# Kernel optimization log

Measured on AMD Instinct MI355X. Metric: run time of the kernel, lower is better.

## Reference

```python
import jax, jax.numpy as jnp
import numpy as np

N_SRC = 100000
N_DST = 100000
E = 500000
D = 128
L = 2


def _sage(x_src, x_dst, e_src, e_dst, W_self, W_neigh, b):
    # DGL SAGEConv('mean'): out = x_dst @ W_self^T + mean_neighbors(x_src) @ W_neigh^T + b
    n_dst = x_dst.shape[0]
    msg_sum = jax.ops.segment_sum(x_src[e_src], e_dst, num_segments=n_dst)  # [n_dst, D]
    deg = jax.ops.segment_sum(jnp.ones((e_dst.shape[0],), x_src.dtype), e_dst, num_segments=n_dst)
    h_neigh = msg_sum / jnp.maximum(deg, 1.0)[:, None]  # isolated nodes -> 0
    return x_dst @ W_self.T + h_neigh @ W_neigh.T + b


def setup_inputs() -> dict:
    key = jax.random.key(0)
    ks = jax.random.split(key, 10)
    s = 1.0 / np.sqrt(D)
    return {
        "x_src": jax.random.normal(ks[0], (N_SRC, D), jnp.float32),
        "x_dst": jax.random.normal(ks[1], (N_DST, D), jnp.float32),
        "e_src": jax.random.randint(ks[2], (E,), 0, N_SRC, jnp.int32),
        "e_dst": jax.random.randint(ks[3], (E,), 0, N_DST, jnp.int32),
        "W_ship_self": jax.random.normal(ks[4], (L, D, D), jnp.float32) * s,
        "W_ship_neigh": jax.random.normal(ks[5], (L, D, D), jnp.float32) * s,
        "b_ship": jnp.zeros((L, D), jnp.float32),
        "W_rev_self": jax.random.normal(ks[6], (L, D, D), jnp.float32) * s,
        "W_rev_neigh": jax.random.normal(ks[7], (L, D, D), jnp.float32) * s,
        "b_rev": jnp.zeros((L, D), jnp.float32),
    }


def reference(x_src, x_dst, e_src, e_dst, W_ship_self, W_ship_neigh, b_ship,
              W_rev_self, W_rev_neigh, b_rev):
    h_s, h_d = x_src, x_dst
    n_layers = W_ship_self.shape[0]
    for l in range(n_layers):
        # ('source','ship','destination'): messages source -> destination
        new_d = _sage(h_s, h_d, e_src, e_dst, W_ship_self[l], W_ship_neigh[l], b_ship[l])
        # ('destination','rev_ship','source'): messages destination -> source
        new_s = _sage(h_d, h_s, e_dst, e_src, W_rev_self[l], W_rev_neigh[l], b_rev[l])
        h_d = jax.nn.relu(new_d)
        h_s = jax.nn.relu(new_s)
        # dropout p=0.0 (eval) -> identity
    return h_s, h_d
```

## Files before the change

### kernel.cpp

```cpp
#include <hip/hip_runtime.h>
#include <hip/hip_bf16.h>

#define NN 100000
#define EDGES 500000
#define DD 128
#define NBKT 196
#define SLACK 3584
#define CHUNK 4096
#define BPD ((EDGES + CHUNK - 1) / CHUNK)

typedef short bf16x8 __attribute__((ext_vector_type(8)));
typedef float f32x4  __attribute__((ext_vector_type(4)));
typedef float f32x2  __attribute__((ext_vector_type(2)));

__device__ __forceinline__ unsigned short f2bf(float f) {
    unsigned u = __float_as_uint(f);
    u += 0x7fffu + ((u >> 16) & 1u);
    return (unsigned short)(u >> 16);
}

__global__ void f2bx_kernel(const float* __restrict__ a, const float* __restrict__ b,
                            unsigned short* __restrict__ oa, unsigned short* __restrict__ ob) {
    const float* in = blockIdx.y ? b : a;
    unsigned short* out = blockIdx.y ? ob : oa;
    int i = blockIdx.x * 256 + threadIdx.x;
    float4 v = ((const float4*)in)[i];
    ushort4 o;
    o.x = f2bf(v.x); o.y = f2bf(v.y); o.z = f2bf(v.z); o.w = f2bf(v.w);
    ((ushort4*)out)[i] = o;
}

__global__ void f2bw_kernel(const float* __restrict__ w0, const float* __restrict__ w1,
                            const float* __restrict__ w2, const float* __restrict__ w3,
                            unsigned short* __restrict__ o0, unsigned short* __restrict__ o1,
                            unsigned short* __restrict__ o2, unsigned short* __restrict__ o3) {
    const float* in; unsigned short* out;
    switch (blockIdx.y) {
        case 0: in = w0; out = o0; break;
        case 1: in = w1; out = o1; break;
        case 2: in = w2; out = o2; break;
        default: in = w3; out = o3; break;
    }
    int i = blockIdx.x * 256 + threadIdx.x;
    float4 v = ((const float4*)in)[i];
    ushort4 o;
    o.x = f2bf(v.x); o.y = f2bf(v.y); o.z = f2bf(v.z); o.w = f2bf(v.w);
    ((ushort4*)out)[i] = o;
}

__global__ __launch_bounds__(256) void bin_scatter_kernel(
    const int* __restrict__ e_src, const int* __restrict__ e_dst,
    int* __restrict__ gcnt,
    unsigned* __restrict__ recbin)
{
    const int dir = blockIdx.y;
    const int t = threadIdx.x;
    const int c0 = blockIdx.x * CHUNK;
    const int nvalid = min(CHUNK, EDGES - c0);
    const int* __restrict__ TGT = dir ? e_src : e_dst;
    const int* __restrict__ PAY = dir ? e_dst : e_src;

    __shared__ int hist[256];
    __shared__ int lbase[256];
    __shared__ int lofs[256];
    __shared__ int scanA[256], scanB[256];
    __shared__ int laddr[CHUNK];
    __shared__ unsigned lrec[CHUNK];

    hist[t] = 0;
    __syncthreads();

    int myb[16], myslot[16];
    unsigned myrec[16];
    #pragma unroll
    for (int j = 0; j < 16; ++j) {
        int e = c0 + j * 256 + t;
        myb[j] = -1;
        if (e < EDGES) {
            int tgt = TGT[e], pay = PAY[e];
            int b = tgt >> 9;
            myb[j] = b;
            myrec[j] = ((unsigned)pay << 9) | (unsigned)(tgt & 511);
            myslot[j] = atomicAdd(&hist[b], 1);
        }
    }
    __syncthreads();
    int cnt = hist[t];
    lbase[t] = (cnt > 0) ? atomicAdd(&gcnt[dir * 256 + t], cnt) : 0;
    scanA[t] = cnt;
    __syncthreads();
    int* pa = scanA; int* pb = scanB;
    for (int d = 1; d < 256; d <<= 1) {
        pb[t] = pa[t] + (t >= d ? pa[t - d] : 0);
        __syncthreads();
        int* tmp = pa; pa = pb; pb = tmp;
    }
    lofs[t] = pa[t] - cnt;
    __syncthreads();
    #pragma unroll
    for (int j = 0; j < 16; ++j) {
        if (myb[j] >= 0) {
            int b = myb[j];
            int pos = lofs[b] + myslot[j];
            int g = lbase[b] + myslot[j];
            lrec[pos] = myrec[j];
            laddr[pos] = (g < SLACK) ? (b * SLACK + g) : -1;
        }
    }
    __syncthreads();
    unsigned* __restrict__ out = recbin + (size_t)dir * NBKT * SLACK;
    #pragma unroll
    for (int j = 0; j < 16; ++j) {
        int i = j * 256 + t;
        if (i < nvalid) {
            int a = laddr[i];
            if (a >= 0) out[a] = lrec[i];
        }
    }
}

__global__ void bucket_scan_kernel(const int* __restrict__ gcnt, int* __restrict__ csr_base) {
    int t = threadIdx.x;
    __shared__ int A[256], B[256];
    for (int dir = 0; dir < 2; ++dir) {
        int c = (t < NBKT) ? min(gcnt[dir * 256 + t], SLACK) : 0;
        A[t] = c;
        __syncthreads();
        int* pa = A; int* pb = B;
        for (int d = 1; d < 256; d <<= 1) {
            pb[t] = pa[t] + (t >= d ? pa[t - d] : 0);
            __syncthreads();
            int* tmp = pa; pa = pb; pb = tmp;
        }
        if (t < NBKT) csr_base[dir * 200 + t] = pa[t] - c;
        if (t == 0)   csr_base[dir * 200 + NBKT] = pa[255];
        __syncthreads();
    }
}

__global__ __launch_bounds__(256) void fine_place_kernel(
    const unsigned* __restrict__ recbin, const int* __restrict__ gcnt,
    const int* __restrict__ csr_base,
    int* __restrict__ rp_dst, int* __restrict__ rp_src,
    float* __restrict__ inv_dst, float* __restrict__ inv_src,
    int* __restrict__ csr_dst, int* __restrict__ csr_src)
{
    const int dir = blockIdx.y;
    const int bkt = blockIdx.x;
    const int t = threadIdx.x;
    int*   __restrict__ rp  = dir ? rp_src  : rp_dst;
    float* __restrict__ inv = dir ? inv_src : inv_dst;
    int*   __restrict__ csr = dir ? csr_src : csr_dst;
    const unsigned* __restrict__ recs = recbin + ((size_t)dir * NBKT + bkt) * SLACK;
    const int cnt = min(gcnt[dir * 256 + bkt], SLACK);
    const int cbase = csr_base[dir * 200 + bkt];
    const int n0 = bkt * 512;

    __shared__ int deg[512];
    __shared__ int sA[512], sB[512];
    __shared__ int cur[512];
    deg[t] = 0; deg[t + 256] = 0;
    __syncthreads();
    for (int i = t; i < cnt; i += 256)
        atomicAdd(&deg[recs[i] & 511u], 1);
    __syncthreads();
    sA[t] = deg[t]; sA[t + 256] = deg[t + 256];
    __syncthreads();
    int* pa = sA; int* pb = sB;
    for (int d = 1; d < 512; d <<= 1) {
        pb[t]       = pa[t]       + (t >= d           ? pa[t - d]       : 0);
        pb[t + 256] = pa[t + 256] + ((t + 256) >= d   ? pa[t + 256 - d] : 0);
        __syncthreads();
        int* tmp = pa; pa = pb; pb = tmp;
    }
    #pragma unroll
    for (int k = 0; k < 2; ++k) {
        int i = t + k * 256;
        int off = pa[i] - deg[i];
        cur[i] = off;
        int node = n0 + i;
        if (node < NN) {
            rp[node] = cbase + off;
            inv[node] = 1.0f / (float)max(deg[i], 1);
        }
    }
    if (bkt == NBKT - 1 && t == 0) rp[NN] = csr_base[dir * 200 + NBKT];
    __syncthreads();
    for (int i = t; i < cnt; i += 256) {
        unsigned r = recs[i];
        int p = atomicAdd(&cur[r & 511u], 1);
        csr[cbase + p] = (int)(r >> 9);
    }
}

__global__ __launch_bounds__(256) void aggregate3_kernel(
    const unsigned short* __restrict__ h0, const int* __restrict__ rp0,
    const int* __restrict__ csr0, unsigned short* __restrict__ ag0,
    const unsigned short* __restrict__ h1, const int* __restrict__ rp1,
    const int* __restrict__ csr1, unsigned short* __restrict__ ag1)
{
    const int dir = blockIdx.y;
    const unsigned short* __restrict__ h = dir ? h1 : h0;
    const int* __restrict__ rp   = dir ? rp1 : rp0;
    const int* __restrict__ csr  = dir ? csr1 : csr0;
    unsigned short* __restrict__ agg = dir ? ag1 : ag0;

    const int t  = blockIdx.x * 256 + threadIdx.x;
    const int g  = t >> 4;
    const int sl = t & 15;

    const int beg = rp[g], end = rp[g + 1];
    const unsigned short* __restrict__ hp = h + sl * 8;

    f32x2 acc[4];
    #pragma unroll
    for (int k = 0; k < 4; ++k) acc[k] = (f32x2){0.f, 0.f};

    int cidx[8];
    #pragma unroll
    for (int j = 0; j < 8; ++j)
        cidx[j] = (beg + j < end) ? csr[beg + j] : -1;

    bf16x8 v[8];
    #pragma unroll
    for (int j = 0; j < 8; ++j)
        if (cidx[j] >= 0)
            v[j] = *(const bf16x8*)(hp + (size_t)cidx[j] * DD);

    #pragma unroll
    for (int j = 0; j < 8; ++j) {
        if (cidx[j] >= 0) {
            const unsigned* pu = (const unsigned*)&v[j];
            #pragma unroll
            for (int k = 0; k < 4; ++k) {
                unsigned u = pu[k];
                acc[k] += (f32x2){__uint_as_float(u << 16),
                                  __uint_as_float(u & 0xffff0000u)};
            }
        }
    }

    for (int i = beg + 8; i < end; ++i) {
        int c = csr[i];
        bf16x8 w = *(const bf16x8*)(hp + (size_t)c * DD);
        const unsigned* pu = (const unsigned*)&w;
        #pragma unroll
        for (int k = 0; k < 4; ++k) {
            unsigned u = pu[k];
            acc[k] += (f32x2){__uint_as_float(u << 16),
                              __uint_as_float(u & 0xffff0000u)};
        }
    }

    const float sc = 1.0f / (float)max(end - beg, 1);
    uint4 ov;
    ov.x = (unsigned)f2bf(acc[0].x * sc) | ((unsigned)f2bf(acc[0].y * sc) << 16);
    ov.y = (unsigned)f2bf(acc[1].x * sc) | ((unsigned)f2bf(acc[1].y * sc) << 16);
    ov.z = (unsigned)f2bf(acc[2].x * sc) | ((unsigned)f2bf(acc[2].y * sc) << 16);
    ov.w = (unsigned)f2bf(acc[3].x * sc) | ((unsigned)f2bf(acc[3].y * sc) << 16);
    *(uint4*)(agg + (size_t)g * DD + sl * 8) = ov;
}

__global__ __launch_bounds__(256, 4) void mfma_gemm7_kernel(
    const unsigned short* __restrict__ Hs0, const unsigned short* __restrict__ Ha0,
    const unsigned short* __restrict__ Ws0, const unsigned short* __restrict__ Wn0,
    const float* __restrict__ bias0, float* __restrict__ outF0, unsigned short* __restrict__ outB0,
    const unsigned short* __restrict__ Hs1, const unsigned short* __restrict__ Ha1,
    const unsigned short* __restrict__ Ws1, const unsigned short* __restrict__ Wn1,
    const float* __restrict__ bias1, float* __restrict__ outF1, unsigned short* __restrict__ outB1,
    int M)
{
    const int dir = blockIdx.y >> 1;
    const int nh  = blockIdx.y & 1;
    const unsigned short* __restrict__ Hself = dir ? Hs1 : Hs0;
    const unsigned short* __restrict__ Hagg  = dir ? Ha1 : Ha0;
    const unsigned short* __restrict__ Wself = dir ? Ws1 : Ws0;
    const unsigned short* __restrict__ Wneigh= dir ? Wn1 : Wn0;
    const float* __restrict__ bias = dir ? bias1 : bias0;
    float* __restrict__ outF = dir ? outF1 : outF0;
    unsigned short* __restrict__ outB = dir ? outB1 : outB0;

    __shared__ __align__(16) unsigned short sW[64 * 256];
    const int tid  = threadIdx.x;
    const int lane = tid & 63;
    const int w    = tid >> 6;
    const int row0 = blockIdx.x * 256;

    #pragma unroll
    for (int i = 0; i < 8; ++i) {
        int q = i * 256 + tid;
        int n = q >> 5, c = q & 31;
        const unsigned short* src = (c < 16) ? (Wself  + (nh * 64 + n) * 128 + c * 8)
                                             : (Wneigh + (nh * 64 + n) * 128 + (c - 16) * 8);
        int d = n * 256 + (c & 24) * 8 + (((c ^ n) & 7) * 8);
        *(uint4*)(sW + d) = *(const uint4*)src;
    }

    const int mbase = w * 64;
    const int l15 = lane & 15;
    const int l4  = lane >> 4;

    int voff[4];
    #pragma unroll
    for (int mt = 0; mt < 4; ++mt) {
        int grow = row0 + mbase + mt * 16 + l15;
        if (grow >= M) grow = M - 1;
        voff[mt] = grow * 128 + l4 * 8;
    }

    f32x4 acc[4][4];
    #pragma unroll
    for (int mt = 0; mt < 4; ++mt)
        #pragma unroll
        for (int nt = 0; nt < 4; ++nt) acc[mt][nt] = (f32x4){0.f, 0.f, 0.f, 0.f};

    __syncthreads();

    bf16x8 a_cur[4], a_nxt[4];
    #pragma unroll
    for (int mt = 0; mt < 4; ++mt) a_cur[mt] = *(const bf16x8*)(Hself + voff[mt]);

    #pragma unroll
    for (int ks = 0; ks < 8; ++ks) {
        if (ks < 7) {
            const int ks1 = ks + 1;
            const int col = (ks1 & 3) * 32;
            const unsigned short* __restrict__ base = (ks1 < 4) ? Hself : Hagg;
            #pragma unroll
            for (int mt = 0; mt < 4; ++mt)
                a_nxt[mt] = *(const bf16x8*)(base + voff[mt] + col);
        }
        const int c = ks * 4 + l4;
        bf16x8 b[4];
        #pragma unroll
        for (int nt = 0; nt < 4; ++nt) {
            int n = nt * 16 + l15;
            b[nt] = *(const bf16x8*)(sW + n * 256 + (c & 24) * 8 + (((c ^ n) & 7) * 8));
        }
        #pragma unroll
        for (int mt = 0; mt < 4; ++mt) {
            acc[mt][0] = __builtin_amdgcn_mfma_f32_16x16x32_bf16(a_cur[mt], b[0], acc[mt][0], 0, 0, 0);
            acc[mt][1] = __builtin_amdgcn_mfma_f32_16x16x32_bf16(a_cur[mt], b[1], acc[mt][1], 0, 0, 0);
            acc[mt][2] = __builtin_amdgcn_mfma_f32_16x16x32_bf16(a_cur[mt], b[2], acc[mt][2], 0, 0, 0);
            acc[mt][3] = __builtin_amdgcn_mfma_f32_16x16x32_bf16(a_cur[mt], b[3], acc[mt][3], 0, 0, 0);
        }
        #pragma unroll
        for (int mt = 0; mt < 4; ++mt) a_cur[mt] = a_nxt[mt];
    }

    #pragma unroll
    for (int nt = 0; nt < 4; ++nt) {
        int col = nh * 64 + nt * 16 + l15;
        float bj = bias[col];
        #pragma unroll
        for (int mt = 0; mt < 4; ++mt) {
            #pragma unroll
            for (int r = 0; r < 4; ++r) {
                int grow = row0 + mbase + mt * 16 + l4 * 4 + r;
                if (grow < M) {
                    float v = fmaxf(acc[mt][nt][r] + bj, 0.f);
                    if (outF) outF[(size_t)grow * 128 + col] = v;
                    else      outB[(size_t)grow * 128 + col] = f2bf(v);
                }
            }
        }
    }
}

extern "C" void kernel_launch(void* const* d_in, const int* in_sizes, int n_in,
                              void* d_out, int out_size, void* d_ws, size_t ws_size,
                              hipStream_t stream) {
    const float* x_src        = (const float*)d_in[0];
    const float* x_dst        = (const float*)d_in[1];
    const int*   e_src        = (const int*)d_in[2];
    const int*   e_dst        = (const int*)d_in[3];
    const float* W_ship_self  = (const float*)d_in[4];
    const float* W_ship_neigh = (const float*)d_in[5];
    const float* b_ship       = (const float*)d_in[6];
    const float* W_rev_self   = (const float*)d_in[7];
    const float* W_rev_neigh  = (const float*)d_in[8];
    const float* b_rev        = (const float*)d_in[9];
    float* out = (float*)d_out;

    char* ws = (char*)d_ws;
    size_t off = 0;
    auto alloc = [&](size_t bytes) {
        char* p = ws + off;
        off = (off + bytes + 255) & ~(size_t)255;
        return p;
    };
    unsigned short* xs_bf  = (unsigned short*)alloc((size_t)NN * DD * 2);
    unsigned short* xd_bf  = (unsigned short*)alloc((size_t)NN * DD * 2);
    unsigned short* xs2_bf = (unsigned short*)alloc((size_t)NN * DD * 2);
    unsigned short* xd2_bf = (unsigned short*)alloc((size_t)NN * DD * 2);
    unsigned short* agg1   = (unsigned short*)alloc((size_t)NN * DD * 2);
    unsigned short* agg2   = (unsigned short*)alloc((size_t)NN * DD * 2);
    unsigned short* Wss_bf = (unsigned short*)alloc(2 * DD * DD * 2);
    unsigned short* Wsn_bf = (unsigned short*)alloc(2 * DD * DD * 2);
    unsigned short* Wrs_bf = (unsigned short*)alloc(2 * DD * DD * 2);
    unsigned short* Wrn_bf = (unsigned short*)alloc(2 * DD * DD * 2);
    int* gcnt = (int*)alloc(2 * 256 * 4);
    int* csr_base = (int*)alloc(2 * 200 * 4);
    unsigned* recbin = (unsigned*)alloc((size_t)2 * NBKT * SLACK * 4);
    int* rp_dst = (int*)alloc((NN + 1) * 4);
    int* rp_src = (int*)alloc((NN + 1) * 4);
    float* inv_dst = (float*)alloc(NN * 4);
    float* inv_src = (float*)alloc(NN * 4);
    int* csr_dst = (int*)alloc(EDGES * 4);
    int* csr_src = (int*)alloc(EDGES * 4);
    (void)ws_size; (void)in_sizes; (void)n_in; (void)out_size;

    hipMemsetAsync(gcnt, 0, 2 * 256 * 4, stream);

    const int xn4 = NN * DD / 4;
    f2bx_kernel<<<dim3(xn4 / 256, 2), 256, 0, stream>>>(x_src, x_dst, xs_bf, xd_bf);
    f2bw_kernel<<<dim3(32, 4), 256, 0, stream>>>(W_ship_self, W_ship_neigh, W_rev_self, W_rev_neigh,
                                                 Wss_bf, Wsn_bf, Wrs_bf, Wrn_bf);

    bin_scatter_kernel<<<dim3(BPD, 2), 256, 0, stream>>>(e_src, e_dst, gcnt, recbin);
    bucket_scan_kernel<<<1, 256, 0, stream>>>(gcnt, csr_base);
    fine_place_kernel<<<dim3(NBKT, 2), 256, 0, stream>>>(recbin, gcnt, csr_base,
        rp_dst, rp_src, inv_dst, inv_src, csr_dst, csr_src);

    float* out_s = out;
    float* out_d = out + (size_t)NN * DD;
    const int gemm_grid = (NN + 255) / 256;
    const int agg_grid  = NN * 16 / 256;

    for (int l = 0; l < 2; ++l) {
        const unsigned short* hs = l ? xs2_bf : xs_bf;
        const unsigned short* hd = l ? xd2_bf : xd_bf;
        aggregate3_kernel<<<dim3(agg_grid, 2), 256, 0, stream>>>(
            hs, rp_dst, csr_dst, agg1,
            hd, rp_src, csr_src, agg2);
        mfma_gemm7_kernel<<<dim3(gemm_grid, 4), 256, 0, stream>>>(
            hd, agg1, Wss_bf + l * DD * DD, Wsn_bf + l * DD * DD, b_ship + l * DD,
            l ? out_d : nullptr, l ? nullptr : xd2_bf,
            hs, agg2, Wrs_bf + l * DD * DD, Wrn_bf + l * DD * DD, b_rev + l * DD,
            l ? out_s : nullptr, l ? nullptr : xs2_bf,
            NN);
    }
}
```

Measured before the change: 449.1 us.

## Store bf16 features in MFMA-tiled layout and widen GEMM blocks to full N

Bf16 feature and aggregate buffers move from row-major to a 16-row tiled layout matching the MFMA A-operand fragment, so each wave loads a contiguous 1KB chunk per K-step. The conversion, aggregation and GEMM epilogue are all updated to this layout. The GEMM now uses 512-thread blocks covering all 128 output columns, which loads the activation tile once instead of twice at the cost of double LDS for weights. The bf16 epilogue writes become scattered 2-byte stores into the tiled layout, which may be less coalesced.

```diff
diff --git a/kernel.cpp b/kernel.cpp
--- a/kernel.cpp
+++ b/kernel.cpp
@@ -9,6 +9,7 @@
 #define CHUNK 4096
 #define BPD ((EDGES + CHUNK - 1) / CHUNK)
 
+
 typedef short bf16x8 __attribute__((ext_vector_type(8)));
 typedef float f32x4  __attribute__((ext_vector_type(4)));
 typedef float f32x2  __attribute__((ext_vector_type(2)));
@@ -23,11 +24,17 @@
                             unsigned short* __restrict__ oa, unsigned short* __restrict__ ob) {
     const float* in = blockIdx.y ? b : a;
     unsigned short* out = blockIdx.y ? ob : oa;
-    int i = blockIdx.x * 256 + threadIdx.x;
-    float4 v = ((const float4*)in)[i];
-    ushort4 o;
-    o.x = f2bf(v.x); o.y = f2bf(v.y); o.z = f2bf(v.z); o.w = f2bf(v.w);
-    ((ushort4*)out)[i] = o;
+    int t = blockIdx.x * 256 + threadIdx.x;
+    int row = t >> 4, sl = t & 15;
+    const float4* src = (const float4*)in + row * 32 + sl * 2;
+    float4 v0 = src[0], v1 = src[1];
+    uint4 o;
+    o.x = (unsigned)f2bf(v0.x) | ((unsigned)f2bf(v0.y) << 16);
+    o.y = (unsigned)f2bf(v0.z) | ((unsigned)f2bf(v0.w) << 16);
+    o.z = (unsigned)f2bf(v1.x) | ((unsigned)f2bf(v1.y) << 16);
+    o.w = (unsigned)f2bf(v1.z) | ((unsigned)f2bf(v1.w) << 16);
+    int boff = (row >> 4) * 2048 + (sl >> 2) * 512 + (sl & 3) * 128 + (row & 15) * 8;
+    *(uint4*)(out + boff) = o;
 }
 
 __global__ void f2bw_kernel(const float* __restrict__ w0, const float* __restrict__ w1,
@@ -193,7 +200,7 @@
     }
 }
 
-__global__ __launch_bounds__(256) void aggregate3_kernel(
+__global__ __launch_bounds__(256) void aggregate4_kernel(
     const unsigned short* __restrict__ h0, const int* __restrict__ rp0,
     const int* __restrict__ csr0, unsigned short* __restrict__ ag0,
     const unsigned short* __restrict__ h1, const int* __restrict__ rp1,
@@ -210,7 +217,8 @@
     const int sl = t & 15;
 
     const int beg = rp[g], end = rp[g + 1];
-    const unsigned short* __restrict__ hp = h + sl * 8;
+    const int koff = (sl >> 2) * 512 + (sl & 3) * 128;
+    const unsigned short* __restrict__ hp = h + koff;
 
     f32x2 acc[4];
     #pragma unroll
@@ -224,8 +232,10 @@
     bf16x8 v[8];
     #pragma unroll
     for (int j = 0; j < 8; ++j)
-        if (cidx[j] >= 0)
-            v[j] = *(const bf16x8*)(hp + (size_t)cidx[j] * DD);
+        if (cidx[j] >= 0) {
+            int c = cidx[j];
+            v[j] = *(const bf16x8*)(hp + (c >> 4) * 2048 + (c & 15) * 8);
+        }
 
     #pragma unroll
     for (int j = 0; j < 8; ++j) {
@@ -242,8 +252,8 @@
 
     for (int i = beg + 8; i < end; ++i) {
         int c = csr[i];
-        bf16x8 w = *(const bf16x8*)(hp + (size_t)c * DD);
-        const unsigned* pu = (const unsigned*)&w;
+        bf16x8 wv = *(const bf16x8*)(hp + (c >> 4) * 2048 + (c & 15) * 8);
+        const unsigned* pu = (const unsigned*)&wv;
         #pragma unroll
         for (int k = 0; k < 4; ++k) {
             unsigned u = pu[k];
@@ -258,10 +268,10 @@
     ov.y = (unsigned)f2bf(acc[1].x * sc) | ((unsigned)f2bf(acc[1].y * sc) << 16);
     ov.z = (unsigned)f2bf(acc[2].x * sc) | ((unsigned)f2bf(acc[2].y * sc) << 16);
     ov.w = (unsigned)f2bf(acc[3].x * sc) | ((unsigned)f2bf(acc[3].y * sc) << 16);
-    *(uint4*)(agg + (size_t)g * DD + sl * 8) = ov;
-}
-
-__global__ __launch_bounds__(256, 4) void mfma_gemm7_kernel(
+    *(uint4*)(agg + (g >> 4) * 2048 + koff + (g & 15) * 8) = ov;
+}
+
+__global__ __launch_bounds__(512, 4) void mfma_gemm8_kernel(
     const unsigned short* __restrict__ Hs0, const unsigned short* __restrict__ Ha0,
     const unsigned short* __restrict__ Ws0, const unsigned short* __restrict__ Wn0,
     const float* __restrict__ bias0, float* __restrict__ outF0, unsigned short* __restrict__ outB0,
@@ -270,8 +280,7 @@
     const float* __restrict__ bias1, float* __restrict__ outF1, unsigned short* __restrict__ outB1,
     int M)
 {
-    const int dir = blockIdx.y >> 1;
-    const int nh  = blockIdx.y & 1;
+    const int dir = blockIdx.y;
     const unsigned short* __restrict__ Hself = dir ? Hs1 : Hs0;
     const unsigned short* __restrict__ Hagg  = dir ? Ha1 : Ha0;
     const unsigned short* __restrict__ Wself = dir ? Ws1 : Ws0;
@@ -280,7 +289,7 @@
     float* __restrict__ outF = dir ? outF1 : outF0;
     unsigned short* __restrict__ outB = dir ? outB1 : outB0;
 
-    __shared__ __align__(16) unsigned short sW[64 * 256];
+    __shared__ __align__(16) unsigned short sW[128 * 256];
     const int tid  = threadIdx.x;
     const int lane = tid & 63;
     const int w    = tid >> 6;
@@ -288,24 +297,26 @@
 
     #pragma unroll
     for (int i = 0; i < 8; ++i) {
-        int q = i * 256 + tid;
+        int q = i * 512 + tid;
         int n = q >> 5, c = q & 31;
-        const unsigned short* src = (c < 16) ? (Wself  + (nh * 64 + n) * 128 + c * 8)
-                                             : (Wneigh + (nh * 64 + n) * 128 + (c - 16) * 8);
+        const unsigned short* src = (c < 16) ? (Wself + n * 128 + c * 8)
+                                             : (Wneigh + n * 128 + (c - 16) * 8);
         int d = n * 256 + (c & 24) * 8 + (((c ^ n) & 7) * 8);
         *(uint4*)(sW + d) = *(const uint4*)src;
     }
 
-    const int mbase = w * 64;
+    const int mbase = (w >> 1) * 64;
+    const int nbase = (w & 1) * 64;
     const int l15 = lane & 15;
     const int l4  = lane >> 4;
-
-    int voff[4];
+    const int MT  = M >> 4;
+
+    int aoff[4];
     #pragma unroll
     for (int mt = 0; mt < 4; ++mt) {
-        int grow = row0 + mbase + mt * 16 + l15;
-        if (grow >= M) grow = M - 1;
-        voff[mt] = grow * 128 + l4 * 8;
+        int rt = ((row0 + mbase) >> 4) + mt;
+        if (rt >= MT) rt = MT - 1;
+        aoff[mt] = rt * 2048 + lane * 8;
     }
 
     f32x4 acc[4][4];
@@ -318,23 +329,23 @@
 
     bf16x8 a_cur[4], a_nxt[4];
     #pragma unroll
-    for (int mt = 0; mt < 4; ++mt) a_cur[mt] = *(const bf16x8*)(Hself + voff[mt]);
+    for (int mt = 0; mt < 4; ++mt) a_cur[mt] = *(const bf16x8*)(Hself + aoff[mt]);
 
     #pragma unroll
     for (int ks = 0; ks < 8; ++ks) {
         if (ks < 7) {
             const int ks1 = ks + 1;
-            const int col = (ks1 & 3) * 32;
+            const int col = (ks1 & 3) * 512;
             const unsigned short* __restrict__ base = (ks1 < 4) ? Hself : Hagg;
             #pragma unroll
             for (int mt = 0; mt < 4; ++mt)
-                a_nxt[mt] = *(const bf16x8*)(base + voff[mt] + col);
+                a_nxt[mt] = *(const bf16x8*)(base + aoff[mt] + col);
         }
         const int c = ks * 4 + l4;
         bf16x8 b[4];
         #pragma unroll
         for (int nt = 0; nt < 4; ++nt) {
-            int n = nt * 16 + l15;
+            int n = nbase + nt * 16 + l15;
             b[nt] = *(const bf16x8*)(sW + n * 256 + (c & 24) * 8 + (((c ^ n) & 7) * 8));
         }
         #pragma unroll
@@ -350,7 +361,7 @@
 
     #pragma unroll
     for (int nt = 0; nt < 4; ++nt) {
-        int col = nh * 64 + nt * 16 + l15;
+        int col = nbase + nt * 16 + l15;
         float bj = bias[col];
         #pragma unroll
         for (int mt = 0; mt < 4; ++mt) {
@@ -359,8 +370,13 @@
                 int grow = row0 + mbase + mt * 16 + l4 * 4 + r;
                 if (grow < M) {
                     float v = fmaxf(acc[mt][nt][r] + bj, 0.f);
-                    if (outF) outF[(size_t)grow * 128 + col] = v;
-                    else      outB[(size_t)grow * 128 + col] = f2bf(v);
+                    if (outF) {
+                        outF[(size_t)grow * 128 + col] = v;
+                    } else {
+                        int bo = (grow >> 4) * 2048 + (col >> 5) * 512
+                               + ((col >> 3) & 3) * 128 + (grow & 15) * 8 + (col & 7);
+                        outB[bo] = f2bf(v);
+                    }
                 }
             }
         }
@@ -412,8 +428,7 @@
 
     hipMemsetAsync(gcnt, 0, 2 * 256 * 4, stream);
 
-    const int xn4 = NN * DD / 4;
-    f2bx_kernel<<<dim3(xn4 / 256, 2), 256, 0, stream>>>(x_src, x_dst, xs_bf, xd_bf);
+    f2bx_kernel<<<dim3(NN * 16 / 256, 2), 256, 0, stream>>>(x_src, x_dst, xs_bf, xd_bf);
     f2bw_kernel<<<dim3(32, 4), 256, 0, stream>>>(W_ship_self, W_ship_neigh, W_rev_self, W_rev_neigh,
                                                  Wss_bf, Wsn_bf, Wrs_bf, Wrn_bf);
 
@@ -430,10 +445,10 @@
     for (int l = 0; l < 2; ++l) {
         const unsigned short* hs = l ? xs2_bf : xs_bf;
         const unsigned short* hd = l ? xd2_bf : xd_bf;
-        aggregate3_kernel<<<dim3(agg_grid, 2), 256, 0, stream>>>(
+        aggregate4_kernel<<<dim3(agg_grid, 2), 256, 0, stream>>>(
             hs, rp_dst, csr_dst, agg1,
             hd, rp_src, csr_src, agg2);
-        mfma_gemm7_kernel<<<dim3(gemm_grid, 4), 256, 0, stream>>>(
+        mfma_gemm8_kernel<<<dim3(gemm_grid, 2), 512, 0, stream>>>(
             hd, agg1, Wss_bf + l * DD * DD, Wsn_bf + l * DD * DD, b_ship + l * DD,
             l ? out_d : nullptr, l ? nullptr : xd2_bf,
             hs, agg2, Wrs_bf + l * DD * DD, Wrn_bf + l * DD * DD, b_rev + l * DD,
```

Measured after the change: 802.8 us. 1.79x slower.
